# Performance work log

Hardware: AMD Instinct MI355X
Metric: run time of the kernel (lower is better)

The kernel has to match this reference:

```python
import jax, jax.numpy as jnp
import numpy as np

DIM = 256
HEADS = 4
HEAD_DIM = DIM // HEADS  # 64
SCALE = (DIM / HEADS) ** -0.5
EPS = 1e-5


def layer_norm(x, g, b):
    mu = jnp.mean(x, axis=-1, keepdims=True)
    var = jnp.mean(jnp.square(x - mu), axis=-1, keepdims=True)
    return (x - mu) * jax.lax.rsqrt(var + EPS) * g + b


def setup_inputs() -> dict:
    key = jax.random.key(0)
    ks = jax.random.split(key, 8)
    B, N, C = 2, 64 * 64, DIM
    H = 4 * DIM  # mlp hidden
    s = lambda fan: 1.0 / np.sqrt(fan)
    return {
        "x": jax.random.normal(ks[0], (B, N, C), jnp.float32),
        "w_qkv": jax.random.normal(ks[1], (C, 3 * C), jnp.float32) * s(C),
        "w_ao": jax.random.normal(ks[2], (C, C), jnp.float32) * s(C),
        "b_ao": jnp.zeros((C,), jnp.float32),
        "g_ao": jnp.ones((C,), jnp.float32),
        "be_ao": jnp.zeros((C,), jnp.float32),
        "g1": jnp.ones((C,), jnp.float32),
        "be1": jnp.zeros((C,), jnp.float32),
        "w_fc1": jax.random.normal(ks[3], (C, H), jnp.float32) * s(C),
        "b_fc1": jnp.zeros((H,), jnp.float32),
        "w_fc2": jax.random.normal(ks[4], (H, C), jnp.float32) * s(H),
        "b_fc2": jnp.zeros((C,), jnp.float32),
        "g2": jnp.ones((C,), jnp.float32),
        "be2": jnp.zeros((C,), jnp.float32),
    }


def reference(x, w_qkv, w_ao, b_ao, g_ao, be_ao, g1, be1,
              w_fc1, b_fc1, w_fc2, b_fc2, g2, be2):
    b, n, c = x.shape
    shortcut = x

    # --- LinearAttention ---
    qkv = x @ w_qkv  # [b, n, 3c]
    qkv = qkv.reshape(b, n, 3, HEADS, HEAD_DIM).transpose(2, 0, 3, 1, 4)  # [3,b,h,n,d]
    q, k, v = qkv[0], qkv[1], qkv[2]
    k = jax.nn.softmax(k, axis=-2)  # softmax over sequence dim
    q = q * SCALE
    context = jnp.einsum('bhid,bhjd->bhij', k, v)   # [b,h,n,n]
    out = jnp.einsum('bhij,bhid->bhjd', context, q)  # [b,h,n,d]
    out = out.reshape(b, n, c)  # faithful to torch reshape (no transpose)
    attn_out = layer_norm(out @ w_ao + b_ao, g_ao, be_ao)

    # --- block residuals ---
    h = shortcut + layer_norm(attn_out, g1, be1)
    mlp = jax.nn.gelu(h @ w_fc1 + b_fc1) @ w_fc2 + b_fc2
    h = h + layer_norm(mlp, g2, be2)
    return shortcut + h
```

## Files before the change

kernel.cpp:

```cpp
#include <hip/hip_runtime.h>

typedef __attribute__((ext_vector_type(8))) short short8;
typedef __attribute__((ext_vector_type(4))) float f32x4;

#define EPSF 1e-5f
#define NSEQ 4096
#define R_TOT 8192

__device__ __forceinline__ float bf2f(unsigned short u){
  union { unsigned int i; float f; } v; v.i = ((unsigned int)u) << 16; return v.f;
}
__device__ __forceinline__ unsigned short f2bf(float f){
  union { float f; unsigned int i; } v; v.f = f;
  unsigned int u = v.i;
  u += 0x7FFFu + ((u >> 16) & 1u);
  return (unsigned short)(u >> 16);
}
__device__ __forceinline__ float wsum(float v){
  #pragma unroll
  for (int o = 32; o > 0; o >>= 1) v += __shfl_xor(v, o, 64);
  return v;
}
__device__ __forceinline__ float gelu_tanh(float x){
  float y = 0.7978845608028654f * (x + 0.044715f * x * x * x);
  float e = __expf(2.0f * y);
  float th = 1.0f - 2.0f / (e + 1.0f);
  return 0.5f * x * (1.0f + th);
}
__device__ __forceinline__ void gload_lds16(const unsigned short* g, unsigned short* l){
  __builtin_amdgcn_global_load_lds(
      (const __attribute__((address_space(1))) unsigned int*)g,
      (__attribute__((address_space(3))) unsigned int*)l, 16, 0, 0);
}

__global__ void k_prep(const float* __restrict__ x, unsigned short* __restrict__ xbf,
                       const float* __restrict__ w_qkv, const float* __restrict__ w_ao,
                       const float* __restrict__ w_fc1, const float* __restrict__ w_fc2,
                       unsigned short* __restrict__ oq, unsigned short* __restrict__ oa,
                       unsigned short* __restrict__ o1, unsigned short* __restrict__ o2)
{
  int bid = blockIdx.x;
  const int t = threadIdx.x;
  if (bid < 2048){
    int i = (bid * 256 + t) * 4;
    float4 v = *(const float4*)(x + i);
    ushort4 o;
    o.x = f2bf(v.x); o.y = f2bf(v.y); o.z = f2bf(v.z); o.w = f2bf(v.w);
    *(ushort4*)(xbf + i) = o;
    return;
  }
  bid -= 2048;
  const float* in; unsigned short* out; int rows, cols, tid;
  if (bid < 48)      { in = w_qkv; out = oq; rows = 256;  cols = 768;  tid = bid; }
  else if (bid < 64) { in = w_ao;  out = oa; rows = 256;  cols = 256;  tid = bid - 48; }
  else if (bid < 128){ in = w_fc1; out = o1; rows = 256;  cols = 1024; tid = bid - 64; }
  else               { in = w_fc2; out = o2; rows = 1024; cols = 256;  tid = bid - 128; }
  const int tC = cols >> 6;
  const int r0 = (tid / tC) * 64, c0 = (tid % tC) * 64;
  __shared__ float tile[64][68];
  const int i = t >> 4, j4 = (t & 15) * 4;
  #pragma unroll
  for (int p = 0; p < 4; p++){
    float4 v = *(const float4*)(in + (size_t)(r0 + i + p * 16) * cols + c0 + j4);
    tile[i + p * 16][j4 + 0] = v.x; tile[i + p * 16][j4 + 1] = v.y;
    tile[i + p * 16][j4 + 2] = v.z; tile[i + p * 16][j4 + 3] = v.w;
  }
  __syncthreads();
  #pragma unroll
  for (int p = 0; p < 4; p++){
    int ci = i + p * 16;
    ushort4 o;
    o.x = f2bf(tile[j4 + 0][ci]); o.y = f2bf(tile[j4 + 1][ci]);
    o.z = f2bf(tile[j4 + 2][ci]); o.w = f2bf(tile[j4 + 3][ci]);
    *(ushort4*)(out + (size_t)(c0 + ci) * rows + r0 + j4) = o;
  }
}

template<int BM, int BN, bool HAS_BIAS, bool DO_GELU, bool OUT_BF16>
__global__ __launch_bounds__(256) void k_gemm(const unsigned short* __restrict__ A,
                       const unsigned short* __restrict__ BT,
                       const float* __restrict__ bias,
                       float* __restrict__ Cf,
                       unsigned short* __restrict__ Cb,
                       int M, int N, int K)
{
  constexpr int BK = 64;
  constexpr int FM = BM / 32, FN = BN / 32;
  __shared__ unsigned short As[2][BM * BK];
  __shared__ unsigned short Bs[2][BN * BK];
  const int t  = threadIdx.x;
  const int l  = t & 63;
  const int w  = t >> 6;
  const int wm = w >> 1, wn = w & 1;
  const int lr = l & 15, kq = l >> 4;
  const int m0 = blockIdx.y * BM, n0 = blockIdx.x * BN;

  f32x4 acc[FM][FN];
  #pragma unroll
  for (int i = 0; i < FM; i++)
    #pragma unroll
    for (int j = 0; j < FN; j++) acc[i][j] = (f32x4){0.f, 0.f, 0.f, 0.f};

  const int crow = l >> 3, ccolE = (l & 7) * 8;
  const int nk = K / BK;

  auto stage = [&](int s, int bsel){
    #pragma unroll
    for (int c = w; c < BM / 8; c += 4)
      gload_lds16(A  + (size_t)(m0 + c * 8 + crow) * K + s * BK + ccolE, &As[bsel][c * 512]);
    #pragma unroll
    for (int c = w; c < BN / 8; c += 4)
      gload_lds16(BT + (size_t)(n0 + c * 8 + crow) * K + s * BK + ccolE, &Bs[bsel][c * 512]);
  };

  stage(0, 0);
  __syncthreads();
  for (int s = 0; s < nk; ++s){
    const int cur = s & 1;
    if (s + 1 < nk) stage(s + 1, cur ^ 1);
    #pragma unroll
    for (int kk = 0; kk < BK; kk += 32){
      short8 af[FM], bfr[FN];
      #pragma unroll
      for (int i = 0; i < FM; i++)
        af[i]  = *(const short8*)&As[cur][(wm * (BM / 2) + i * 16 + lr) * 64 + kk + kq * 8];
      #pragma unroll
      for (int j = 0; j < FN; j++)
        bfr[j] = *(const short8*)&Bs[cur][(wn * (BN / 2) + j * 16 + lr) * 64 + kk + kq * 8];
      #pragma unroll
      for (int i = 0; i < FM; i++)
        #pragma unroll
        for (int j = 0; j < FN; j++)
          acc[i][j] = __builtin_amdgcn_mfma_f32_16x16x32_bf16(af[i], bfr[j], acc[i][j], 0, 0, 0);
    }
    __syncthreads();
  }

  const int row0 = m0 + wm * (BM / 2);
  const int col0 = n0 + wn * (BN / 2);
  #pragma unroll
  for (int i = 0; i < FM; i++){
    #pragma unroll
    for (int j = 0; j < FN; j++){
      #pragma unroll
      for (int r = 0; r < 4; r++){
        int row = row0 + i * 16 + kq * 4 + r;
        int col = col0 + j * 16 + lr;
        float v = acc[i][j][r];
        if (HAS_BIAS) v += bias[col];
        if (DO_GELU)  v = gelu_tanh(v);
        if (OUT_BF16) Cb[(size_t)row * N + col] = f2bf(v);
        else          Cf[(size_t)row * N + col] = v;
      }
    }
  }
}

#define NPAD 72
__global__ __launch_bounds__(256) void k_msum(const unsigned short* __restrict__ qkv,
                                              float* __restrict__ Spart,
                                              float* __restrict__ dsum_part)
{
  __shared__ unsigned short kT[64 * NPAD];
  __shared__ unsigned short qT[80 * NPAD];
  const int t = threadIdx.x;
  const int sl = blockIdx.x;
  const int bh = blockIdx.y;
  const int b = bh >> 2, h = bh & 3;
  const int e4 = (t & 15) * 4;
  const int col = (t >> 4) * 4;
  {
    int n = sl * 64 + col;
    const unsigned short* rp = qkv + (size_t)(b * NSEQ + n) * 768 + h * 64 + e4;
    ushort4 q0 = *(const ushort4*)(rp);
    ushort4 q1 = *(const ushort4*)(rp + 768);
    ushort4 q2 = *(const ushort4*)(rp + 1536);
    ushort4 q3 = *(const ushort4*)(rp + 2304);
    ushort4 k0 = *(const ushort4*)(rp + 256);
    ushort4 k1 = *(const ushort4*)(rp + 1024);
    ushort4 k2 = *(const ushort4*)(rp + 1792);
    ushort4 k3 = *(const ushort4*)(rp + 2560);
    ushort4 w;
    w.x = q0.x; w.y = q1.x; w.z = q2.x; w.w = q3.x; *(ushort4*)&qT[(e4+0)*NPAD + col] = w;
    w.x = q0.y; w.y = q1.y; w.z = q2.y; w.w = q3.y; *(ushort4*)&qT[(e4+1)*NPAD + col] = w;
    w.x = q0.z; w.y = q1.z; w.z = q2.z; w.w = q3.z; *(ushort4*)&qT[(e4+2)*NPAD + col] = w;
    w.x = q0.w; w.y = q1.w; w.z = q2.w; w.w = q3.w; *(ushort4*)&qT[(e4+3)*NPAD + col] = w;
    w.x = f2bf(__expf(bf2f(k0.x))); w.y = f2bf(__expf(bf2f(k1.x)));
    w.z = f2bf(__expf(bf2f(k2.x))); w.w = f2bf(__expf(bf2f(k3.x)));
    *(ushort4*)&kT[(e4+0)*NPAD + col] = w;
    w.x = f2bf(__expf(bf2f(k0.y))); w.y = f2bf(__expf(bf2f(k1.y)));
    w.z = f2bf(__expf(bf2f(k2.y))); w.w = f2bf(__expf(bf2f(k3.y)));
    *(ushort4*)&kT[(e4+1)*NPAD + col] = w;
    w.x = f2bf(__expf(bf2f(k0.z))); w.y = f2bf(__expf(bf2f(k1.z)));
    w.z = f2bf(__expf(bf2f(k2.z))); w.w = f2bf(__expf(bf2f(k3.z)));
    *(ushort4*)&kT[(e4+2)*NPAD + col] = w;
    w.x = f2bf(__expf(bf2f(k0.w))); w.y = f2bf(__expf(bf2f(k1.w)));
    w.z = f2bf(__expf(bf2f(k2.w))); w.w = f2bf(__expf(bf2f(k3.w)));
    *(ushort4*)&kT[(e4+3)*NPAD + col] = w;
  }
  if (t < 16){
    ushort4 ones; ones.x = 0x3F80; ones.y = 0x3F80; ones.z = 0x3F80; ones.w = 0x3F80;
    *(ushort4*)&qT[64 * NPAD + t * 4] = ones;
  }
  __syncthreads();
  const int w4 = t >> 6, lr = t & 15, kq = (t >> 4) & 3;
  f32x4 acc[5];
  #pragma unroll
  for (int j = 0; j < 5; ++j) acc[j] = (f32x4){0.f, 0.f, 0.f, 0.f};
  #pragma unroll
  for (int ks = 0; ks < 2; ++ks){
    int nc = ks * 32 + kq * 8;
    short8 af = *(const short8*)&kT[(w4 * 16 + lr) * NPAD + nc];
    #pragma unroll
    for (int j = 0; j < 5; ++j){
      short8 bf = *(const short8*)&qT[(j * 16 + lr) * NPAD + nc];
      acc[j] = __builtin_amdgcn_mfma_f32_16x16x32_bf16(af, bf, acc[j], 0, 0, 0);
    }
  }
  float* sp = Spart + ((size_t)sl * 8 + bh) * 4096;
  #pragma unroll
  for (int j = 0; j < 4; ++j)
    #pragma unroll
    for (int r = 0; r < 4; ++r)
      sp[(w4 * 16 + kq * 4 + r) * 64 + j * 16 + lr] = acc[j][r];
  if (lr == 0){
    float* dp = dsum_part + (sl * 8 + bh) * 64;
    #pragma unroll
    for (int r = 0; r < 4; ++r) dp[w4 * 16 + kq * 4 + r] = acc[4][r];
  }
}

__global__ void k_mreduce(const float* __restrict__ Spart, const float* __restrict__ dsum_part,
                          float* __restrict__ Mm, float* __restrict__ dsumb){
  int bid = blockIdx.x, t = threadIdx.x;
  if (bid < 128){
    int idx = bid * 256 + t;
    float s = 0.f;
    #pragma unroll 8
    for (int sl = 0; sl < 64; ++sl) s += Spart[(size_t)sl * 32768 + idx];
    Mm[idx] = s;
  } else {
    int oi = (bid - 128) * 256 + t;
    float s = 0.f;
    #pragma unroll 8
    for (int sl = 0; sl < 64; ++sl) s += dsum_part[sl * 512 + oi];
    dsumb[oi] = s;
  }
}

__global__ __launch_bounds__(256) void k_projvm_dln(
    const unsigned short* __restrict__ qkv,
    const float* __restrict__ Mm, const float* __restrict__ dsumb,
    const unsigned short* __restrict__ waoT,
    const float* __restrict__ bias, const float* __restrict__ x,
    const float* __restrict__ g_ao, const float* __restrict__ be_ao,
    const float* __restrict__ g1, const float* __restrict__ be1,
    unsigned short* __restrict__ hbf, float* __restrict__ sxh)
{
  __shared__ __align__(16) char smem[16896 + 16384 + 8192 + 65536];
  unsigned short* As   = (unsigned short*)smem;
  unsigned short* vlds = (unsigned short*)(smem + 16896);
  unsigned short* mt   = (unsigned short*)(smem + 16896 + 16384);
  unsigned short* Bs0  = (unsigned short*)(smem + 41472);
  float*          yt   = (float*)(smem + 41472);

  const int t = threadIdx.x, l = t & 63, w = t >> 6;
  const int lr = l & 15, kq = l >> 4;
  const int m0 = blockIdx.x * 32;
  const int b = m0 >> 12, h = (m0 >> 10) & 3;
  const int bh = b * 4 + h;
  const int n0 = (m0 & 1023) * 4;
  const int crow = l >> 3, ccolE = (l & 7) * 8;

  const unsigned short* vbase = qkv + (size_t)(b * NSEQ + n0) * 768 + 512 + h * 64;
  #pragma unroll
  for (int c = w; c < 16; c += 4)
    gload_lds16(vbase + (size_t)(c * 8 + crow) * 768 + ccolE, vlds + c * 512);
  #pragma unroll
  for (int c = w; c < 32; c += 4)
    gload_lds16(waoT + (size_t)(c * 8 + crow) * 256 + ccolE, Bs0 + c * 512);
  {
    int e = t >> 2, d0 = (t & 3) * 16;
    float rdn = 0.125f / dsumb[bh * 64 + e];
    const float* mp = Mm + (size_t)bh * 4096 + e * 64 + d0;
    #pragma unroll
    for (int i = 0; i < 16; i += 4){
      float4 mv = *(const float4*)(mp + i);
      mt[(d0 + i + 0) * 64 + e] = f2bf(mv.x * rdn);
      mt[(d0 + i + 1) * 64 + e] = f2bf(mv.y * rdn);
      mt[(d0 + i + 2) * 64 + e] = f2bf(mv.z * rdn);
      mt[(d0 + i + 3) * 64 + e] = f2bf(mv.w * rdn);
    }
  }
  __syncthreads();
  {
    f32x4 vacc[2][4];
    #pragma unroll
    for (int i = 0; i < 2; i++)
      #pragma unroll
      for (int j = 0; j < 4; j++) vacc[i][j] = (f32x4){0.f, 0.f, 0.f, 0.f};
    #pragma unroll
    for (int kk = 0; kk < 64; kk += 32){
      short8 vf[2], mf[4];
      #pragma unroll
      for (int i = 0; i < 2; i++)
        vf[i] = *(const short8*)&vlds[((w * 2 + i) * 16 + lr) * 64 + kk + kq * 8];
      #pragma unroll
      for (int j = 0; j < 4; j++)
        mf[j] = *(const short8*)&mt[(j * 16 + lr) * 64 + kk + kq * 8];
      #pragma unroll
      for (int i = 0; i < 2; i++)
        #pragma unroll
        for (int j = 0; j < 4; j++)
          vacc[i][j] = __builtin_amdgcn_mfma_f32_16x16x32_bf16(vf[i], mf[j], vacc[i][j], 0, 0, 0);
    }
    #pragma unroll
    for (int i = 0; i < 2; i++)
      #pragma unroll
      for (int j = 0; j < 4; j++)
        #pragma unroll
        for (int r = 0; r < 4; r++)
          As[((w * 2 + i) * 4 + kq) * 264 + r * 64 + j * 16 + lr] = f2bf(vacc[i][j][r]);
  }
  __syncthreads();
  f32x4 acc[2][4];
  #pragma unroll
  for (int i = 0; i < 2; i++)
    #pragma unroll
    for (int j = 0; j < 4; j++) acc[i][j] = (f32x4){0.f, 0.f, 0.f, 0.f};
  for (int s = 0; s < 4; ++s){
    const int cur = s & 1;
    if (s + 1 < 4){
      unsigned short* bnxt = Bs0 + (cur ^ 1) * 16384;
      #pragma unroll
      for (int c = w; c < 32; c += 4)
        gload_lds16(waoT + (size_t)(c * 8 + crow) * 256 + (s + 1) * 64 + ccolE,
                    bnxt + c * 512);
    }
    const unsigned short* bcur = Bs0 + cur * 16384;
    #pragma unroll
    for (int kk = 0; kk < 64; kk += 32){
      short8 af[2], bfr[4];
      #pragma unroll
      for (int i = 0; i < 2; i++)
        af[i] = *(const short8*)&As[(i * 16 + lr) * 264 + s * 64 + kk + kq * 8];
      #pragma unroll
      for (int j = 0; j < 4; j++)
        bfr[j] = *(const short8*)&bcur[(w * 64 + j * 16 + lr) * 64 + kk + kq * 8];
      #pragma unroll
      for (int i = 0; i < 2; i++)
        #pragma unroll
        for (int j = 0; j < 4; j++)
          acc[i][j] = __builtin_amdgcn_mfma_f32_16x16x32_bf16(af[i], bfr[j], acc[i][j], 0, 0, 0);
    }
    __syncthreads();
  }
  #pragma unroll
  for (int i = 0; i < 2; i++)
    #pragma unroll
    for (int j = 0; j < 4; j++){
      float bv = bias[w * 64 + j * 16 + lr];
      #pragma unroll
      for (int r = 0; r < 4; r++)
        yt[(i * 16 + kq * 4 + r) * 260 + w * 64 + j * 16 + lr] = acc[i][j][r] + bv;
    }
  __syncthreads();
  const int gl = t & 63;
  #pragma unroll
  for (int rp = 0; rp < 8; rp++){
    int row = rp * 4 + (t >> 6);
    float4 v = *(const float4*)(yt + row * 260 + gl * 4);
    float mu = wsum(v.x + v.y + v.z + v.w) * 0.00390625f;
    float dx = v.x - mu, dy = v.y - mu, dz = v.z - mu, dw = v.w - mu;
    float rstd = rsqrtf(wsum(dx*dx + dy*dy + dz*dz + dw*dw) * 0.00390625f + EPSF);
    float4 ga = *(const float4*)(g_ao + gl * 4);
    float4 ba = *(const float4*)(be_ao + gl * 4);
    float zx = dx * rstd * ga.x + ba.x, zy = dy * rstd * ga.y + ba.y;
    float zz = dz * rstd * ga.z + ba.z, zw = dw * rstd * ga.w + ba.w;
    float mu2 = wsum(zx + zy + zz + zw) * 0.00390625f;
    float ex = zx - mu2, ey = zy - mu2, ez = zz - mu2, ew = zw - mu2;
    float rstd2 = rsqrtf(wsum(ex*ex + ey*ey + ez*ez + ew*ew) * 0.00390625f + EPSF);
    float4 gb = *(const float4*)(g1 + gl * 4);
    float4 bb = *(const float4*)(be1 + gl * 4);
    size_t off = (size_t)(m0 + row) * 256 + gl * 4;
    float4 xr = *(const float4*)(x + off);
    float hx = xr.x + ex * rstd2 * gb.x + bb.x;
    float hy = xr.y + ey * rstd2 * gb.y + bb.y;
    float hz = xr.z + ez * rstd2 * gb.z + bb.z;
    float hw = xr.w + ew * rstd2 * gb.w + bb.w;
    ushort4 hb; hb.x = f2bf(hx); hb.y = f2bf(hy); hb.z = f2bf(hz); hb.w = f2bf(hw);
    *(ushort4*)(hbf + off) = hb;
    float4 sv = {xr.x + hx, xr.y + hy, xr.z + hz, xr.w + hw};
    *(float4*)(sxh + off) = sv;
  }
}

__global__ __launch_bounds__(256) void k_fc2_ln(
    const unsigned short* __restrict__ A, const unsigned short* __restrict__ BT,
    const float* __restrict__ bias, const float* __restrict__ sxh,
    const float* __restrict__ g2, const float* __restrict__ be2,
    float* __restrict__ out)
{
  constexpr int K = 1024;
  __shared__ __align__(16) char smem[4096 + 65536];
  unsigned short* As0 = (unsigned short*)smem;
  unsigned short* Bs0 = (unsigned short*)(smem + 4096);
  float* yt = (float*)(smem + 4096);
  const int t = threadIdx.x, l = t & 63, w = t >> 6;
  const int lr = l & 15, kq = l >> 4;
  const int m0 = blockIdx.x * 16;
  const int crow = l >> 3, ccolE = (l & 7) * 8;
  f32x4 acc[4];
  #pragma unroll
  for (int j = 0; j < 4; j++) acc[j] = (f32x4){0.f, 0.f, 0.f, 0.f};

  auto stage = [&](int s, int bsel){
    if (w < 2)
      gload_lds16(A + (size_t)(m0 + w * 8 + crow) * K + s * 64 + ccolE,
                  As0 + bsel * 1024 + w * 512);
    unsigned short* bdst = Bs0 + bsel * 16384;
    #pragma unroll
    for (int c = w; c < 32; c += 4)
      gload_lds16(BT + (size_t)(c * 8 + crow) * K + s * 64 + ccolE, bdst + c * 512);
  };

  stage(0, 0);
  __syncthreads();
  for (int s = 0; s < 16; ++s){
    const int cur = s & 1;
    if (s + 1 < 16) stage(s + 1, cur ^ 1);
    const unsigned short* acur = As0 + cur * 1024;
    const unsigned short* bcur = Bs0 + cur * 16384;
    #pragma unroll
    for (int kk = 0; kk < 64; kk += 32){
      short8 af = *(const short8*)&acur[lr * 64 + kk + kq * 8];
      #pragma unroll
      for (int j = 0; j < 4; j++){
        short8 bfr = *(const short8*)&bcur[(w * 64 + j * 16 + lr) * 64 + kk + kq * 8];
        acc[j] = __builtin_amdgcn_mfma_f32_16x16x32_bf16(af, bfr, acc[j], 0, 0, 0);
      }
    }
    __syncthreads();
  }
  #pragma unroll
  for (int j = 0; j < 4; j++){
    float bv = bias[w * 64 + j * 16 + lr];
    #pragma unroll
    for (int r = 0; r < 4; r++)
      yt[(kq * 4 + r) * 260 + w * 64 + j * 16 + lr] = acc[j][r] + bv;
  }
  __syncthreads();
  const int gl = t & 63;
  #pragma unroll
  for (int rp = 0; rp < 4; rp++){
    int row = rp * 4 + (t >> 6);
    float4 v = *(const float4*)(yt + row * 260 + gl * 4);
    float mu = wsum(v.x + v.y + v.z + v.w) * 0.00390625f;
    float dx = v.x - mu, dy = v.y - mu, dz = v.z - mu, dw = v.w - mu;
    float rstd = rsqrtf(wsum(dx*dx + dy*dy + dz*dz + dw*dw) * 0.00390625f + EPSF);
    float4 g = *(const float4*)(g2 + gl * 4);
    float4 be = *(const float4*)(be2 + gl * 4);
    size_t off = (size_t)(m0 + row) * 256 + gl * 4;
    float4 sv = *(const float4*)(sxh + off);
    float4 o;
    o.x = sv.x + dx * rstd * g.x + be.x;
    o.y = sv.y + dy * rstd * g.y + be.y;
    o.z = sv.z + dz * rstd * g.z + be.z;
    o.w = sv.w + dw * rstd * g.w + be.w;
    *(float4*)(out + off) = o;
  }
}

extern "C" void kernel_launch(void* const* d_in, const int* in_sizes, int n_in,
                              void* d_out, int out_size, void* d_ws, size_t ws_size,
                              hipStream_t stream)
{
  const float* x     = (const float*)d_in[0];
  const float* w_qkv = (const float*)d_in[1];
  const float* w_ao  = (const float*)d_in[2];
  const float* b_ao  = (const float*)d_in[3];
  const float* g_ao  = (const float*)d_in[4];
  const float* be_ao = (const float*)d_in[5];
  const float* g1    = (const float*)d_in[6];
  const float* be1   = (const float*)d_in[7];
  const float* w_fc1 = (const float*)d_in[8];
  const float* b_fc1 = (const float*)d_in[9];
  const float* w_fc2 = (const float*)d_in[10];
  const float* b_fc2 = (const float*)d_in[11];
  const float* g2    = (const float*)d_in[12];
  const float* be2   = (const float*)d_in[13];
  float* out = (float*)d_out;
  char* ws = (char*)d_ws;

  unsigned short* qkv   = (unsigned short*)(ws + 0);
  unsigned short* xbf   = (unsigned short*)(ws + 12582912);
  unsigned short* wqkvT = (unsigned short*)(ws + 16777216);
  unsigned short* waoT  = (unsigned short*)(ws + 17170432);
  unsigned short* wfc1T = (unsigned short*)(ws + 17301504);
  unsigned short* wfc2T = (unsigned short*)(ws + 17825792);
  float* Spart = (float*)(ws + 18350080);
  float* dsum_part = (float*)(ws + 26738688);
  float* Mm    = (float*)(ws + 26869760);
  float* dsumb = (float*)(ws + 27000832);
  float* sxh   = (float*)(ws + 27004928);
  unsigned short* mlp1 = (unsigned short*)(ws + 35393536);

  k_prep<<<2240, 256, 0, stream>>>(x, xbf, w_qkv, w_ao, w_fc1, w_fc2,
                                   wqkvT, waoT, wfc1T, wfc2T);

  k_gemm<128, 128, false, false, true><<<dim3(6, 64), 256, 0, stream>>>(
      xbf, wqkvT, nullptr, nullptr, qkv, R_TOT, 768, 256);

  k_msum<<<dim3(64, 8), 256, 0, stream>>>(qkv, Spart, dsum_part);
  k_mreduce<<<130, 256, 0, stream>>>(Spart, dsum_part, Mm, dsumb);

  k_projvm_dln<<<256, 256, 0, stream>>>(qkv, Mm, dsumb, waoT, b_ao, x,
                                        g_ao, be_ao, g1, be1, xbf, sxh);

  k_gemm<128, 128, true, true, true><<<dim3(8, 64), 256, 0, stream>>>(
      xbf, wfc1T, b_fc1, nullptr, mlp1, R_TOT, 1024, 256);

  k_fc2_ln<<<512, 256, 0, stream>>>(mlp1, wfc2T, b_fc2, sxh, g2, be2, out);
}
```

Baseline: 77.74 us.

## Fold partial-sum reduction into projection kernel and halve msum slices

k_msum now processes two 64-row chunks per block, so the grid drops from 64 to 32 sequence slices and half as many partial matrices are written. The separate k_mreduce kernel is removed. Each k_projvm_dln block sums the 32 partials for its (b,h) directly while building its M tile. This saves a kernel launch and a global round trip, but every projection block now redundantly reads 32 partial slices from global memory, and msum has less parallelism.

```diff
diff --git a/kernel.cpp b/kernel.cpp
--- a/kernel.cpp
+++ b/kernel.cpp
@@ -169,8 +169,14 @@
   const int b = bh >> 2, h = bh & 3;
   const int e4 = (t & 15) * 4;
   const int col = (t >> 4) * 4;
-  {
-    int n = sl * 64 + col;
+  const int w4 = t >> 6, lr = t & 15, kq = (t >> 4) & 3;
+
+  f32x4 acc[5];
+  #pragma unroll
+  for (int j = 0; j < 5; ++j) acc[j] = (f32x4){0.f, 0.f, 0.f, 0.f};
+
+  for (int ch = 0; ch < 2; ++ch){
+    int n = sl * 128 + ch * 64 + col;
     const unsigned short* rp = qkv + (size_t)(b * NSEQ + n) * 768 + h * 64 + e4;
     ushort4 q0 = *(const ushort4*)(rp);
     ushort4 q1 = *(const ushort4*)(rp + 768);
@@ -180,6 +186,7 @@
     ushort4 k1 = *(const ushort4*)(rp + 1024);
     ushort4 k2 = *(const ushort4*)(rp + 1792);
     ushort4 k3 = *(const ushort4*)(rp + 2560);
+    if (ch) __syncthreads();
     ushort4 w;
     w.x = q0.x; w.y = q1.x; w.z = q2.x; w.w = q3.x; *(ushort4*)&qT[(e4+0)*NPAD + col] = w;
     w.x = q0.y; w.y = q1.y; w.z = q2.y; w.w = q3.y; *(ushort4*)&qT[(e4+1)*NPAD + col] = w;
@@ -197,24 +204,20 @@
     w.x = f2bf(__expf(bf2f(k0.w))); w.y = f2bf(__expf(bf2f(k1.w)));
     w.z = f2bf(__expf(bf2f(k2.w))); w.w = f2bf(__expf(bf2f(k3.w)));
     *(ushort4*)&kT[(e4+3)*NPAD + col] = w;
-  }
-  if (t < 16){
-    ushort4 ones; ones.x = 0x3F80; ones.y = 0x3F80; ones.z = 0x3F80; ones.w = 0x3F80;
-    *(ushort4*)&qT[64 * NPAD + t * 4] = ones;
-  }
-  __syncthreads();
-  const int w4 = t >> 6, lr = t & 15, kq = (t >> 4) & 3;
-  f32x4 acc[5];
-  #pragma unroll
-  for (int j = 0; j < 5; ++j) acc[j] = (f32x4){0.f, 0.f, 0.f, 0.f};
-  #pragma unroll
-  for (int ks = 0; ks < 2; ++ks){
-    int nc = ks * 32 + kq * 8;
-    short8 af = *(const short8*)&kT[(w4 * 16 + lr) * NPAD + nc];
-    #pragma unroll
-    for (int j = 0; j < 5; ++j){
-      short8 bf = *(const short8*)&qT[(j * 16 + lr) * NPAD + nc];
-      acc[j] = __builtin_amdgcn_mfma_f32_16x16x32_bf16(af, bf, acc[j], 0, 0, 0);
+    if (ch == 0 && t < 16){
+      ushort4 ones; ones.x = 0x3F80; ones.y = 0x3F80; ones.z = 0x3F80; ones.w = 0x3F80;
+      *(ushort4*)&qT[64 * NPAD + t * 4] = ones;
+    }
+    __syncthreads();
+    #pragma unroll
+    for (int ks = 0; ks < 2; ++ks){
+      int nc = ks * 32 + kq * 8;
+      short8 af = *(const short8*)&kT[(w4 * 16 + lr) * NPAD + nc];
+      #pragma unroll
+      for (int j = 0; j < 5; ++j){
+        short8 bf = *(const short8*)&qT[(j * 16 + lr) * NPAD + nc];
+        acc[j] = __builtin_amdgcn_mfma_f32_16x16x32_bf16(af, bf, acc[j], 0, 0, 0);
+      }
     }
   }
   float* sp = Spart + ((size_t)sl * 8 + bh) * 4096;
@@ -230,27 +233,9 @@
   }
 }
 
-__global__ void k_mreduce(const float* __restrict__ Spart, const float* __restrict__ dsum_part,
-                          float* __restrict__ Mm, float* __restrict__ dsumb){
-  int bid = blockIdx.x, t = threadIdx.x;
-  if (bid < 128){
-    int idx = bid * 256 + t;
-    float s = 0.f;
-    #pragma unroll 8
-    for (int sl = 0; sl < 64; ++sl) s += Spart[(size_t)sl * 32768 + idx];
-    Mm[idx] = s;
-  } else {
-    int oi = (bid - 128) * 256 + t;
-    float s = 0.f;
-    #pragma unroll 8
-    for (int sl = 0; sl < 64; ++sl) s += dsum_part[sl * 512 + oi];
-    dsumb[oi] = s;
-  }
-}
-
 __global__ __launch_bounds__(256) void k_projvm_dln(
     const unsigned short* __restrict__ qkv,
-    const float* __restrict__ Mm, const float* __restrict__ dsumb,
+    const float* __restrict__ Spart, const float* __restrict__ dsum_part,
     const unsigned short* __restrict__ waoT,
     const float* __restrict__ bias, const float* __restrict__ x,
     const float* __restrict__ g_ao, const float* __restrict__ be_ao,
@@ -281,11 +266,18 @@
     gload_lds16(waoT + (size_t)(c * 8 + crow) * 256 + ccolE, Bs0 + c * 512);
   {
     int e = t >> 2, d0 = (t & 3) * 16;
-    float rdn = 0.125f / dsumb[bh * 64 + e];
-    const float* mp = Mm + (size_t)bh * 4096 + e * 64 + d0;
+    float dn = 0.f;
+    #pragma unroll 8
+    for (int sl = 0; sl < 32; ++sl) dn += dsum_part[(sl * 8 + bh) * 64 + e];
+    float rdn = 0.125f / dn;
     #pragma unroll
     for (int i = 0; i < 16; i += 4){
-      float4 mv = *(const float4*)(mp + i);
+      float4 mv = {0.f, 0.f, 0.f, 0.f};
+      #pragma unroll 8
+      for (int sl = 0; sl < 32; ++sl){
+        float4 p = *(const float4*)(Spart + ((size_t)sl * 8 + bh) * 4096 + e * 64 + d0 + i);
+        mv.x += p.x; mv.y += p.y; mv.z += p.z; mv.w += p.w;
+      }
       mt[(d0 + i + 0) * 64 + e] = f2bf(mv.x * rdn);
       mt[(d0 + i + 1) * 64 + e] = f2bf(mv.y * rdn);
       mt[(d0 + i + 2) * 64 + e] = f2bf(mv.z * rdn);
@@ -499,11 +491,9 @@
   unsigned short* wfc1T = (unsigned short*)(ws + 17301504);
   unsigned short* wfc2T = (unsigned short*)(ws + 17825792);
   float* Spart = (float*)(ws + 18350080);
-  float* dsum_part = (float*)(ws + 26738688);
-  float* Mm    = (float*)(ws + 26869760);
-  float* dsumb = (float*)(ws + 27000832);
-  float* sxh   = (float*)(ws + 27004928);
-  unsigned short* mlp1 = (unsigned short*)(ws + 35393536);
+  float* dsum_part = (float*)(ws + 22544384);
+  float* sxh   = (float*)(ws + 22609920);
+  unsigned short* mlp1 = (unsigned short*)(ws + 30998528);
 
   k_prep<<<2240, 256, 0, stream>>>(x, xbf, w_qkv, w_ao, w_fc1, w_fc2,
                                    wqkvT, waoT, wfc1T, wfc2T);
@@ -511,10 +501,9 @@
   k_gemm<128, 128, false, false, true><<<dim3(6, 64), 256, 0, stream>>>(
       xbf, wqkvT, nullptr, nullptr, qkv, R_TOT, 768, 256);
 
-  k_msum<<<dim3(64, 8), 256, 0, stream>>>(qkv, Spart, dsum_part);
-  k_mreduce<<<130, 256, 0, stream>>>(Spart, dsum_part, Mm, dsumb);
-
-  k_projvm_dln<<<256, 256, 0, stream>>>(qkv, Mm, dsumb, waoT, b_ao, x,
+  k_msum<<<dim3(32, 8), 256, 0, stream>>>(qkv, Spart, dsum_part);
+
+  k_projvm_dln<<<256, 256, 0, stream>>>(qkv, Spart, dsum_part, waoT, b_ao, x,
                                         g_ao, be_ao, g1, be1, xbf, sxh);
 
   k_gemm<128, 128, true, true, true><<<dim3(8, 64), 256, 0, stream>>>(
```

Result: slower. 90.12 us (+15.9%).
